# Performance work log

Hardware: AMD Instinct MI355X
Metric: run time of the kernel (lower is better)

The kernel has to match this reference:

```python
import jax, jax.numpy as jnp
import numpy as np

EPS = 1e-5

def conv1x1(x, w, b=None):
    # x: (B,C,H,W), w: (O,C)
    y = jnp.einsum('bchw,oc->bohw', x, w)
    if b is not None:
        y = y + b[None, :, None, None]
    return y

def bn(x, g, b):
    # torch BatchNorm2d training-mode: biased var over (B,H,W)
    mean = jnp.mean(x, axis=(0, 2, 3), keepdims=True)
    var = jnp.var(x, axis=(0, 2, 3), keepdims=True)
    xn = (x - mean) * jax.lax.rsqrt(var + EPS)
    return xn * g[None, :, None, None] + b[None, :, None, None]

def setup_inputs() -> dict:
    key = jax.random.key(0)
    ks = jax.random.split(key, 8)
    B, C, H, W = 4, 256, 128, 128
    C8 = C // 8
    s = 1.0 / np.sqrt(C)
    return {
        'x': jax.random.normal(ks[0], (B, C, H, W), jnp.float32),
        'w1': jax.random.normal(ks[1], (C, C), jnp.float32) * s,
        'g1': jnp.ones((C,), jnp.float32), 'b1': jnp.zeros((C,), jnp.float32),
        'wq': jax.random.normal(ks[2], (C8, C), jnp.float32) * s,
        'bq': jnp.zeros((C8,), jnp.float32),
        'wk': jax.random.normal(ks[3], (C8, C), jnp.float32) * s,
        'bk': jnp.zeros((C8,), jnp.float32),
        'wv': jax.random.normal(ks[4], (C, C), jnp.float32) * s,
        'bv': jnp.zeros((C,), jnp.float32),
        'gamma_att': jax.random.normal(ks[5], (1,), jnp.float32),
        'g2': jnp.ones((C,), jnp.float32), 'b2': jnp.zeros((C,), jnp.float32),
        'w3': jax.random.normal(ks[6], (C, C), jnp.float32) * s,
        'g3': jnp.ones((C,), jnp.float32), 'b3': jnp.zeros((C,), jnp.float32),
    }

def att(h, wq, bq, wk, bk, wv, bv, gamma_att):
    B, C, Hh, Ww = h.shape
    N = Hh * Ww
    q = conv1x1(h, wq, bq).reshape(B, -1, N)          # (B,C8,N)
    k = conv1x1(h, wk, bk).reshape(B, -1, N)          # (B,C8,N)
    v = conv1x1(h, wv, bv).reshape(B, C, N)           # (B,C,N)
    energy = jnp.einsum('bdi,bdj->bij', q, k)         # (B,N,N): q^T k
    attn = jax.nn.softmax(energy, axis=-1)
    out = jnp.einsum('bcj,bij->bci', v, attn)         # out[b,c,i]=sum_j v[c,j]*attn[i,j]
    out = out.reshape(B, C, Hh, Ww)
    return gamma_att[0] * out + h

def reference(x, w1, g1, b1, wq, bq, wk, bk, wv, bv, gamma_att, g2, b2, w3, g3, b3):
    B, C, H, W = x.shape
    shortcut = x  # sk=True (dim==dim_out, no downsample)
    h = jax.nn.relu(bn(conv1x1(x, w1), g1, b1))                       # net1
    h = jax.image.resize(h, (B, C, H // 2, W // 2), method='bilinear')  # align_corners=False
    h = att(h, wq, bq, wk, bk, wv, bv, gamma_att)                     # net2: ATT
    h = jax.nn.relu(bn(h, g2, b2))                                    # net2: BN+ReLU (Identity pool)
    h = jax.image.resize(h, (B, C, H, W), method='bilinear')          # stride==1 upsample x2
    h = bn(conv1x1(h, w3), g3, b3)                                    # net3
    return jax.nn.relu(h + shortcut)
```

## Files before the change

### kernel.cpp

```cpp
#include <hip/hip_runtime.h>
#include <hip/hip_bf16.h>

#define EPS_BN 1e-5f

typedef short bf16x8 __attribute__((ext_vector_type(8)));
typedef float f32x4 __attribute__((ext_vector_type(4)));

__device__ __forceinline__ unsigned short f2bf(float f) {
    __hip_bfloat16 h = __float2bfloat16(f);
    return __builtin_bit_cast(unsigned short, h);
}
__device__ __forceinline__ float bf2f(unsigned short u) {
    return __builtin_bit_cast(float, (unsigned)u << 16);
}

template<int BM, int MODE>
__global__ __launch_bounds__(256) void gemm_mfma(
    const unsigned short* __restrict__ Wb,
    const unsigned short* __restrict__ Xt,
    const float* __restrict__ bias,
    unsigned short* __restrict__ Y,
    int P, int O)
{
    const int tid = threadIdx.x;
    const int w = tid >> 6, l = tid & 63;
    const int b = blockIdx.z;
    const int p0 = blockIdx.x * 128;
    const int o0 = blockIdx.y * BM;
    const int lr = l & 15, lk = l >> 4;
    const int srow = l >> 2, sq = l & 3;

    __shared__ unsigned short Al[BM * 40];
    __shared__ unsigned short Bl[128 * 40];

    constexpr int WC = (BM == 32) ? 4 : 2;
    constexpr int MT = (BM == 128) ? 4 : 2;
    constexpr int NT = (WC == 2) ? 4 : 2;
    const int wr = w / WC, wc = w % WC;
    const int osub = wr * MT * 16, psub = wc * NT * 16;

    f32x4 acc[MT][NT];
#pragma unroll
    for (int i = 0; i < MT; i++)
#pragma unroll
        for (int j = 0; j < NT; j++) acc[i][j] = (f32x4){0.f, 0.f, 0.f, 0.f};

    const unsigned short* Xb = Xt + (size_t)b * P * 256;
    const int ar0 = w * 16, ar1 = w * 16 + 64;
    const int br0 = w * 16, br1 = w * 16 + 64;

    const unsigned short* pB0 = Xb + (size_t)(p0 + br0 + srow) * 256 + sq * 8;
    const unsigned short* pB1 = Xb + (size_t)(p0 + br1 + srow) * 256 + sq * 8;
    const unsigned short* pA0 = Wb + (size_t)(o0 + ar0 + srow) * 256 + sq * 8;
    const unsigned short* pA1 = Wb + (size_t)(o0 + ar1 + srow) * 256 + sq * 8;
    unsigned short* BlW0 = &Bl[(br0 + srow) * 40 + sq * 8];
    unsigned short* BlW1 = &Bl[(br1 + srow) * 40 + sq * 8];
    unsigned short* AlW0 = &Al[(ar0 + srow) * 40 + sq * 8];
    unsigned short* AlW1 = &Al[(ar1 + srow) * 40 + sq * 8];

    uint4 vb0, vb1, va0, va1;
#define G_LOADS                                                     \
    vb0 = *(const uint4*)pB0; pB0 += 32;                            \
    vb1 = *(const uint4*)pB1; pB1 += 32;                            \
    if (ar0 < BM) { va0 = *(const uint4*)pA0; pA0 += 32; }          \
    if (ar1 < BM) { va1 = *(const uint4*)pA1; pA1 += 32; }

    G_LOADS
    for (int k0 = 0; k0 < 256; k0 += 32) {
        __syncthreads();
        *(uint4*)BlW0 = vb0;
        *(uint4*)BlW1 = vb1;
        if (ar0 < BM) *(uint4*)AlW0 = va0;
        if (ar1 < BM) *(uint4*)AlW1 = va1;
        __syncthreads();
        if (k0 < 224) { G_LOADS }
        bf16x8 af[MT], bfr[NT];
#pragma unroll
        for (int i = 0; i < MT; i++) {
            int row = osub + i * 16 + lr;
            af[i] = *(const bf16x8*)&Al[row * 40 + lk * 8];
        }
#pragma unroll
        for (int j = 0; j < NT; j++) {
            int row = psub + j * 16 + lr;
            bfr[j] = *(const bf16x8*)&Bl[row * 40 + lk * 8];
        }
#pragma unroll
        for (int i = 0; i < MT; i++)
#pragma unroll
            for (int j = 0; j < NT; j++)
                acc[i][j] = __builtin_amdgcn_mfma_f32_16x16x32_bf16(af[i], bfr[j], acc[i][j], 0, 0, 0);
    }
#undef G_LOADS

    if (MODE == 1) {
#pragma unroll
        for (int i = 0; i < MT; i++) {
            int ob = o0 + osub + i * 16 + lk * 4;
#pragma unroll
            for (int j = 0; j < NT; j++) {
                int p = p0 + psub + j * 16 + lr;
                ushort4 pk;
                pk.x = f2bf(acc[i][j][0] + bias[ob + 0]);
                pk.y = f2bf(acc[i][j][1] + bias[ob + 1]);
                pk.z = f2bf(acc[i][j][2] + bias[ob + 2]);
                pk.w = f2bf(acc[i][j][3] + bias[ob + 3]);
                *(ushort4*)&Y[((size_t)b * P + p) * O + ob] = pk;
            }
        }
    } else {
#pragma unroll
        for (int i = 0; i < MT; i++)
#pragma unroll
            for (int r = 0; r < 4; r++) {
                int o = o0 + osub + i * 16 + lk * 4 + r;
                float bs = bias ? bias[o] : 0.f;
#pragma unroll
                for (int j = 0; j < NT; j++) {
                    int p = p0 + psub + j * 16 + lr;
                    Y[((size_t)(b * 256 + o)) * P + p] = f2bf(acc[i][j][r] + bs);
                }
            }
    }
}

__global__ __launch_bounds__(256) void transpose_cvt(
    const float* __restrict__ src, unsigned short* __restrict__ dst, int P)
{
    __shared__ float t[64][65];
    const int tid = threadIdx.x;
    const int p0 = blockIdx.x * 64, c0 = blockIdx.y * 64, b = blockIdx.z;
    const float* sb = src + ((size_t)b * 256 + c0) * P + p0;
#pragma unroll
    for (int i = 0; i < 16; i++) {
        int r = (tid >> 6) + 4 * i;
        int c = tid & 63;
        t[c][r] = sb[(size_t)r * P + c];
    }
    __syncthreads();
#pragma unroll
    for (int i = 0; i < 8; i++) {
        int pr = (tid >> 5) + 8 * i;
        int cc = (tid & 31) * 2;
        unsigned pk = ((unsigned)f2bf(t[pr][cc + 1]) << 16) | f2bf(t[pr][cc]);
        *(unsigned*)&dst[((size_t)b * P + p0 + pr) * 256 + c0 + cc] = pk;
    }
}

__global__ void cvt_weights(const float* __restrict__ w1, const float* __restrict__ wq,
                            const float* __restrict__ wk, const float* __restrict__ wv,
                            const float* __restrict__ w3,
                            const float* __restrict__ bq, const float* __restrict__ bk,
                            unsigned short* o1, unsigned short* oqk,
                            unsigned short* ov, unsigned short* o3, float* obqk)
{
    int i = blockIdx.x * 256 + threadIdx.x;
    if (i < 65536) { o1[i] = f2bf(w1[i]); ov[i] = f2bf(wv[i]); o3[i] = f2bf(w3[i]); }
    if (i < 16384) oqk[i] = f2bf(i < 8192 ? wq[i] : wk[i - 8192]);
    if (i < 64)    obqk[i] = i < 32 ? bq[i] : bk[i - 32];
}

__global__ __launch_bounds__(256) void channel_stats_bf16(
    const unsigned short* __restrict__ Y, float* __restrict__ psum,
    float* __restrict__ psumsq, int Pn)
{
    const int o = blockIdx.x, b = blockIdx.y;
    const unsigned short* p = Y + ((size_t)b * 256 + o) * Pn;
    float s = 0.f, s2 = 0.f;
    for (int i = threadIdx.x * 8; i < Pn; i += 2048) {
        uint4 v = *(const uint4*)&p[i];
        unsigned uu[4] = {v.x, v.y, v.z, v.w};
#pragma unroll
        for (int k = 0; k < 4; k++) {
            float a = __builtin_bit_cast(float, uu[k] << 16);
            float c = __builtin_bit_cast(float, uu[k] & 0xffff0000u);
            s += a + c; s2 += a * a + c * c;
        }
    }
#pragma unroll
    for (int off = 32; off; off >>= 1) {
        s  += __shfl_down(s, off);
        s2 += __shfl_down(s2, off);
    }
    __shared__ float ws1[4], ws2[4];
    int lane = threadIdx.x & 63, w = threadIdx.x >> 6;
    if (lane == 0) { ws1[w] = s; ws2[w] = s2; }
    __syncthreads();
    if (threadIdx.x == 0) {
        float ts = 0.f, ts2 = 0.f;
#pragma unroll
        for (int k = 0; k < 4; k++) { ts += ws1[k]; ts2 += ws2[k]; }
        psum[(size_t)b * 256 + o] = ts;
        psumsq[(size_t)b * 256 + o] = ts2;
    }
}

__global__ __launch_bounds__(256) void stats_pmajor(
    const float* __restrict__ Y, float* __restrict__ psum, float* __restrict__ psumsq)
{
    const int chunk = blockIdx.x, b = blockIdx.y, c = threadIdx.x;
    const float* base = Y + ((size_t)b * 4096 + chunk * 128) * 256 + c;
    float s = 0.f, s2 = 0.f;
    for (int i = 0; i < 128; i++) { float v = base[(size_t)i * 256]; s += v; s2 += v * v; }
    psum[((size_t)b * 32 + chunk) * 256 + c] = s;
    psumsq[((size_t)b * 32 + chunk) * 256 + c] = s2;
}

__global__ void bn_finalize(const float* __restrict__ psum, const float* __restrict__ psumsq,
                            const float* __restrict__ g, const float* __restrict__ bb,
                            float* __restrict__ scale, float* __restrict__ shift,
                            float invN, int NP)
{
    int o = threadIdx.x;
    float s = 0.f, s2 = 0.f;
    for (int k = 0; k < NP; k++) { s += psum[k * 256 + o]; s2 += psumsq[k * 256 + o]; }
    float mean = s * invN;
    float var  = s2 * invN - mean * mean;
    float r = rsqrtf(var + EPS_BN);
    float sc = g[o] * r;
    scale[o] = sc;
    shift[o] = bb[o] - mean * sc;
}

__device__ __forceinline__ int dtaps(int u, int* j, float* w) {
    if (u == 0)  { j[0]=0;   j[1]=1;   j[2]=2;   w[0]=3.f/7.f; w[1]=3.f/7.f; w[2]=1.f/7.f; return 3; }
    if (u == 63) { j[0]=125; j[1]=126; j[2]=127; w[0]=1.f/7.f; w[1]=3.f/7.f; w[2]=3.f/7.f; return 3; }
    j[0]=2*u-1; j[1]=2*u; j[2]=2*u+1; j[3]=2*u+2;
    w[0]=0.125f; w[1]=0.375f; w[2]=0.375f; w[3]=0.125f; return 4;
}

__global__ __launch_bounds__(256) void bnrelu_down(
    const unsigned short* __restrict__ y1, const float* __restrict__ scale,
    const float* __restrict__ shift, float* __restrict__ h)
{
    int i = blockIdx.x * 256 + threadIdx.x;
    int o = blockIdx.y, b = blockIdx.z;
    int y2 = i >> 6, x2 = i & 63;
    const unsigned short* base = y1 + ((size_t)(b * 256 + o)) * 16384;
    float sc = scale[o], sh = shift[o];
    int jy[4]; float wy[4]; int ny = dtaps(y2, jy, wy);
    int jx[4]; float wx[4]; int nx = dtaps(x2, jx, wx);
    float acc = 0.f;
    for (int a = 0; a < ny; a++) {
        const unsigned short* row = base + jy[a] * 128;
        for (int c = 0; c < nx; c++) {
            float v = fmaxf(fmaf(sc, bf2f(row[jx[c]]), sh), 0.f);
            acc += wy[a] * wx[c] * v;
        }
    }
    h[((size_t)(b * 256 + o)) * 4096 + i] = acc;
}

__global__ __launch_bounds__(512) void attn_partial(
    const unsigned short* __restrict__ qkT, const unsigned short* __restrict__ vb,
    unsigned short* __restrict__ accP, float2* __restrict__ mzP)
{
    const int s = blockIdx.y;
    const int b = blockIdx.z;
    const int i0 = blockIdx.x * 128;
    const int tid = threadIdx.x;
    const int w = tid >> 6, l = tid & 63;
    const int wr = w >> 1, wc = w & 1;
    const int lr = l & 15, lk = l >> 4;

    __shared__ unsigned short Vl[256 * 64];
    __shared__ unsigned short Pl[4][32 * 68];

    const unsigned short* qkTb = qkT + (size_t)b * 4096 * 64;
    bf16x8 qf[2];
#pragma unroll
    for (int i = 0; i < 2; i++)
        qf[i] = *(const bf16x8*)&qkTb[(size_t)(i0 + wr * 32 + i * 16 + lr) * 64 + lk * 8];

    f32x4 acc[2][8];
#pragma unroll
    for (int i = 0; i < 2; i++)
#pragma unroll
        for (int c = 0; c < 8; c++) acc[i][c] = (f32x4){0.f, 0.f, 0.f, 0.f};
    float m[2][4], zp[2][4];
#pragma unroll
    for (int i = 0; i < 2; i++)
#pragma unroll
        for (int r = 0; r < 4; r++) { m[i][r] = -1e30f; zp[i][r] = 0.f; }

    const int jbase = s * 1024;
    const unsigned short* kPtr = qkTb + (size_t)(jbase + lr) * 64 + 32 + lk * 8;
    const unsigned short* vPtr =
        vb + (size_t)b * 256 * 4096 + (size_t)(w * 32 + (l >> 3)) * 4096 + jbase + (l & 7) * 8;
    unsigned short* Pw = Pl[wr];

    uint4 kfr[4], vreg[4];
#pragma unroll
    for (int jt = 0; jt < 4; jt++) kfr[jt] = *(const uint4*)(kPtr + jt * 1024);
    kPtr += 4096;
#pragma unroll
    for (int it = 0; it < 4; it++) vreg[it] = *(const uint4*)(vPtr + it * 32768);

    for (int t = 0; t < 16; t++) {
        __syncthreads();
#pragma unroll
        for (int it = 0; it < 4; it++) {
            int ch = w * 32 + it * 8 + (l >> 3);
            *(uint4*)&Vl[ch * 64 + (((l & 7) ^ (ch & 7)) * 8)] = vreg[it];
        }
        __syncthreads();
        if (t < 15) {
            vPtr += 64;
#pragma unroll
            for (int it = 0; it < 4; it++) vreg[it] = *(const uint4*)(vPtr + it * 32768);
        }

#pragma unroll
        for (int i = 0; i < 2; i++) {
            f32x4 sv[4];
#pragma unroll
            for (int jt = 0; jt < 4; jt++)
                sv[jt] = __builtin_amdgcn_mfma_f32_16x16x32_bf16(
                    qf[i], __builtin_bit_cast(bf16x8, kfr[jt]), (f32x4){0.f,0.f,0.f,0.f}, 0, 0, 0);
            float tml[4];
            bool trig = false;
#pragma unroll
            for (int r = 0; r < 4; r++) {
                tml[r] = fmaxf(fmaxf(sv[0][r], sv[1][r]), fmaxf(sv[2][r], sv[3][r]));
                trig |= (tml[r] > m[i][r] + 10.0f);
            }
            if (__any(trig)) {
                float corr[4];
#pragma unroll
                for (int r = 0; r < 4; r++) {
                    float tm = tml[r];
#pragma unroll
                    for (int off = 1; off < 16; off <<= 1) tm = fmaxf(tm, __shfl_xor(tm, off));
                    float mo = m[i][r];
                    float mn = fmaxf(mo, tm);
                    corr[r] = __expf(mo - mn);
                    m[i][r] = mn;
                    float ps = 0.f;
#pragma unroll
                    for (int jt = 0; jt < 4; jt++) {
                        float p = __expf(sv[jt][r] - mn);
                        ps += p;
                        Pw[(i * 16 + lk * 4 + r) * 68 + lr + jt * 16] = f2bf(p);
                    }
                    zp[i][r] = zp[i][r] * corr[r] + ps;
                }
#pragma unroll
                for (int c = 0; c < 8; c++)
#pragma unroll
                    for (int r = 0; r < 4; r++) acc[i][c][r] *= corr[r];
            } else {
#pragma unroll
                for (int r = 0; r < 4; r++) {
                    float mn = m[i][r];
                    float ps = 0.f;
#pragma unroll
                    for (int jt = 0; jt < 4; jt++) {
                        float p = __expf(sv[jt][r] - mn);
                        ps += p;
                        Pw[(i * 16 + lk * 4 + r) * 68 + lr + jt * 16] = f2bf(p);
                    }
                    zp[i][r] += ps;
                }
            }
        }

        if (t < 15) {
#pragma unroll
            for (int jt = 0; jt < 4; jt++) kfr[jt] = *(const uint4*)(kPtr + jt * 1024);
            kPtr += 4096;
        }

#pragma unroll
        for (int kc = 0; kc < 2; kc++) {
            bf16x8 pa[2];
#pragma unroll
            for (int i = 0; i < 2; i++)
                pa[i] = *(const bf16x8*)&Pw[(i * 16 + lr) * 68 + (kc * 4 + lk) * 8];
#pragma unroll
            for (int ct = 0; ct < 8; ct++) {
                int ch = wc * 128 + ct * 16 + lr;
                bf16x8 vf = *(const bf16x8*)&Vl[ch * 64 + (((kc * 4 + lk) ^ (lr & 7)) * 8)];
#pragma unroll
                for (int i = 0; i < 2; i++)
                    acc[i][ct] = __builtin_amdgcn_mfma_f32_16x16x32_bf16(pa[i], vf, acc[i][ct], 0, 0, 0);
            }
        }
    }

    float zs[2][4];
#pragma unroll
    for (int i = 0; i < 2; i++)
#pragma unroll
        for (int r = 0; r < 4; r++) {
            float zz = zp[i][r];
#pragma unroll
            for (int off = 1; off < 16; off <<= 1) zz += __shfl_xor(zz, off);
            zs[i][r] = zz;
        }
    const size_t rbase0 = (size_t)(b * 4 + s) * 4096 + i0;
    if (wc == 0 && lr == 0) {
#pragma unroll
        for (int i = 0; i < 2; i++)
#pragma unroll
            for (int r = 0; r < 4; r++)
                mzP[rbase0 + wr * 32 + i * 16 + lk * 4 + r] = make_float2(m[i][r], zs[i][r]);
    }

    float* Eb = (float*)Vl;
    __syncthreads();
#pragma unroll
    for (int h = 0; h < 4; h++) {
        if (wr == h) {
#pragma unroll
            for (int i = 0; i < 2; i++)
#pragma unroll
                for (int ct = 0; ct < 8; ct++)
#pragma unroll
                    for (int r = 0; r < 4; r++)
                        Eb[(i * 16 + lk * 4 + r) * 256 + wc * 128 + ct * 16 + lr] = acc[i][ct][r];
        }
        __syncthreads();
        unsigned short* dst = accP + (rbase0 + h * 32) * 256;
#pragma unroll
        for (int q = 0; q < 4; q++) {
            float4 v = ((const float4*)Eb)[tid + q * 512];
            ushort4 pk = { f2bf(v.x), f2bf(v.y), f2bf(v.z), f2bf(v.w) };
            *(ushort4*)&dst[(tid + q * 512) * 4] = pk;
        }
        __syncthreads();
    }
}

__global__ __launch_bounds__(256) void attn_combine(
    const unsigned short* __restrict__ accP, const float2* __restrict__ mzP,
    const unsigned short* __restrict__ hst, const float* __restrict__ gamma_p,
    float* __restrict__ h2t)
{
    const int b = blockIdx.y, ch = threadIdx.x;
    const float gamma = gamma_p[0];
    for (int rr = 0; rr < 8; rr++) {
        int row = blockIdx.x * 8 + rr;
        float2 mz[4];
#pragma unroll
        for (int s = 0; s < 4; s++) mz[s] = mzP[(size_t)(b * 4 + s) * 4096 + row];
        float M = fmaxf(fmaxf(mz[0].x, mz[1].x), fmaxf(mz[2].x, mz[3].x));
        float Z = 0.f, a = 0.f;
#pragma unroll
        for (int s = 0; s < 4; s++) {
            float wgt = __expf(mz[s].x - M);
            Z += wgt * mz[s].y;
            a += wgt * bf2f(accP[((size_t)(b * 4 + s) * 4096 + row) * 256 + ch]);
        }
        size_t off = ((size_t)b * 4096 + row) * 256 + ch;
        h2t[off] = gamma * a / Z + bf2f(hst[off]);
    }
}

__global__ __launch_bounds__(256) void upsample_bnrelu(
    const float* __restrict__ h2t, const float* __restrict__ scale,
    const float* __restrict__ shift, unsigned short* __restrict__ upn)
{
    const int b = blockIdx.y, c = threadIdx.x;
    const float* basep = h2t + ((size_t)b * 4096) * 256 + c;
    float sc = scale[c], sh = shift[c];
    for (int pp = 0; pp < 16; pp++) {
        int p = blockIdx.x * 16 + pp;
        int y = p >> 7, x = p & 127;
        float fy = 0.5f * y - 0.25f, fx = 0.5f * x - 0.25f;
        float fiy = floorf(fy), fix = floorf(fx);
        float wy = fy - fiy, wx = fx - fix;
        int iy = (int)fiy, ix = (int)fix;
        int iy0 = max(iy, 0), iy1 = min(iy + 1, 63);
        int ix0 = max(ix, 0), ix1 = min(ix + 1, 63);
        float v00 = fmaxf(fmaf(sc, basep[(size_t)(iy0 * 64 + ix0) * 256], sh), 0.f);
        float v01 = fmaxf(fmaf(sc, basep[(size_t)(iy0 * 64 + ix1) * 256], sh), 0.f);
        float v10 = fmaxf(fmaf(sc, basep[(size_t)(iy1 * 64 + ix0) * 256], sh), 0.f);
        float v11 = fmaxf(fmaf(sc, basep[(size_t)(iy1 * 64 + ix1) * 256], sh), 0.f);
        float r0 = (1.f - wy) * ((1.f - wx) * v00 + wx * v01)
                 + wy * ((1.f - wx) * v10 + wx * v11);
        upn[((size_t)b * 16384 + p) * 256 + c] = f2bf(r0);
    }
}

__global__ __launch_bounds__(256) void final_add_relu(
    const unsigned short* __restrict__ y3, const float* __restrict__ scale,
    const float* __restrict__ shift, const float* __restrict__ x,
    float* __restrict__ outp)
{
    size_t e = ((size_t)blockIdx.x * 256 + threadIdx.x) * 4;
    int c = (int)((e >> 14) & 255);
    ushort4 yv = *(const ushort4*)&y3[e];
    float4 xv = *(const float4*)&x[e];
    float sc = scale[c], sh = shift[c];
    float4 o;
    o.x = fmaxf(fmaf(sc, bf2f(yv.x), sh) + xv.x, 0.f);
    o.y = fmaxf(fmaf(sc, bf2f(yv.y), sh) + xv.y, 0.f);
    o.z = fmaxf(fmaf(sc, bf2f(yv.z), sh) + xv.z, 0.f);
    o.w = fmaxf(fmaf(sc, bf2f(yv.w), sh) + xv.w, 0.f);
    *(float4*)&outp[e] = o;
}

extern "C" void kernel_launch(void* const* d_in, const int* in_sizes, int n_in,
                              void* d_out, int out_size, void* d_ws, size_t ws_size,
                              hipStream_t stream)
{
    const float* x     = (const float*)d_in[0];
    const float* w1    = (const float*)d_in[1];
    const float* g1    = (const float*)d_in[2];
    const float* b1    = (const float*)d_in[3];
    const float* wq    = (const float*)d_in[4];
    const float* bq    = (const float*)d_in[5];
    const float* wk    = (const float*)d_in[6];
    const float* bk    = (const float*)d_in[7];
    const float* wv    = (const float*)d_in[8];
    const float* bv    = (const float*)d_in[9];
    const float* gamma = (const float*)d_in[10];
    const float* g2    = (const float*)d_in[11];
    const float* b2    = (const float*)d_in[12];
    const float* w3    = (const float*)d_in[13];
    const float* g3    = (const float*)d_in[14];
    const float* b3    = (const float*)d_in[15];
    float* out = (float*)d_out;

    char* wsb = (char*)d_ws;
    unsigned short* y1b = (unsigned short*)wsb;
    unsigned short* xt  = (unsigned short*)(wsb + ((size_t)32 << 20));
    unsigned short* accPb = (unsigned short*)wsb;
    float* hs   = (float*)(wsb + ((size_t)64 << 20));
    unsigned short* vbb = (unsigned short*)(wsb + ((size_t)80 << 20));
    unsigned short* hst = (unsigned short*)(wsb + ((size_t)88 << 20));
    unsigned short* qkT = (unsigned short*)(wsb + ((size_t)96 << 20));
    unsigned short* w1b = (unsigned short*)(wsb + ((size_t)98 << 20));
    unsigned short* wvb  = w1b + 65536;
    unsigned short* w3b  = wvb + 65536;
    unsigned short* wqkb = w3b + 65536;
    float* bqk = (float*)(wqkb + 16384);
    float2* mzP = (float2*)(wsb + ((size_t)98 << 20) + ((size_t)512 << 10));
    float* psum   = (float*)(wsb + ((size_t)99 << 20));
    float* psumsq = psum + 32768;
    float* sc1 = psumsq + 32768; float* sh1 = sc1 + 256;
    float* sc2 = sh1 + 256;      float* sh2 = sc2 + 256;
    float* sc3 = sh2 + 256;      float* sh3 = sc3 + 256;
    unsigned short* y3b = y1b;
    unsigned short* upn = xt;
    float* h2t = hs;

    cvt_weights<<<256, 256, 0, stream>>>(w1, wq, wk, wv, w3, bq, bk,
                                         w1b, wqkb, wvb, w3b, bqk);
    transpose_cvt<<<dim3(256, 4, 4), 256, 0, stream>>>(x, xt, 16384);

    gemm_mfma<128, 2><<<dim3(128, 2, 4), 256, 0, stream>>>(w1b, xt, nullptr, y1b, 16384, 256);
    channel_stats_bf16<<<dim3(256, 4), 256, 0, stream>>>(y1b, psum, psumsq, 16384);
    bn_finalize<<<1, 256, 0, stream>>>(psum, psumsq, g1, b1, sc1, sh1, 1.f / 65536.f, 4);
    bnrelu_down<<<dim3(16, 256, 4), 256, 0, stream>>>(y1b, sc1, sh1, hs);
    transpose_cvt<<<dim3(64, 4, 4), 256, 0, stream>>>(hs, hst, 4096);

    gemm_mfma<64, 1><<<dim3(32, 1, 4), 256, 0, stream>>>(wqkb, hst, bqk, qkT, 4096, 64);
    gemm_mfma<128, 2><<<dim3(32, 2, 4), 256, 0, stream>>>(wvb, hst, bv, vbb, 4096, 256);
    attn_partial<<<dim3(32, 4, 4), 512, 0, stream>>>(qkT, vbb, accPb, mzP);
    attn_combine<<<dim3(512, 4), 256, 0, stream>>>(accPb, mzP, hst, gamma, h2t);

    stats_pmajor<<<dim3(32, 4), 256, 0, stream>>>(h2t, psum, psumsq);
    bn_finalize<<<1, 256, 0, stream>>>(psum, psumsq, g2, b2, sc2, sh2, 1.f / 16384.f, 128);
    upsample_bnrelu<<<dim3(1024, 4), 256, 0, stream>>>(h2t, sc2, sh2, upn);

    gemm_mfma<128, 2><<<dim3(128, 2, 4), 256, 0, stream>>>(w3b, upn, nullptr, y3b, 16384, 256);
    channel_stats_bf16<<<dim3(256, 4), 256, 0, stream>>>(y3b, psum, psumsq, 16384);
    bn_finalize<<<1, 256, 0, stream>>>(psum, psumsq, g3, b3, sc3, sh3, 1.f / 65536.f, 4);
    final_add_relu<<<16384, 256, 0, stream>>>(y3b, sc3, sh3, x, out);
}
```

Baseline: 403.3 us.

## Fuse attention combine with BN stats, store h2 as bf16, vectorize P writes

```diff
diff --git a/kernel.cpp b/kernel.cpp
--- a/kernel.cpp
+++ b/kernel.cpp
@@ -14,7 +14,7 @@
     return __builtin_bit_cast(float, (unsigned)u << 16);
 }
 
-template<int BM, int MODE>
+template<int BM, int MODE, int PERM>
 __global__ __launch_bounds__(256) void gemm_mfma(
     const unsigned short* __restrict__ Wb,
     const unsigned short* __restrict__ Xt,
@@ -118,7 +118,8 @@
 #pragma unroll
                 for (int j = 0; j < NT; j++) {
                     int p = p0 + psub + j * 16 + lr;
-                    Y[((size_t)(b * 256 + o)) * P + p] = f2bf(acc[i][j][r] + bs);
+                    int p2 = PERM ? ((p & ~63) | ((p & 15) * 4 + ((p >> 4) & 3))) : p;
+                    Y[((size_t)(b * 256 + o)) * P + p2] = f2bf(acc[i][j][r] + bs);
                 }
             }
     }
@@ -193,17 +194,6 @@
         psum[(size_t)b * 256 + o] = ts;
         psumsq[(size_t)b * 256 + o] = ts2;
     }
-}
-
-__global__ __launch_bounds__(256) void stats_pmajor(
-    const float* __restrict__ Y, float* __restrict__ psum, float* __restrict__ psumsq)
-{
-    const int chunk = blockIdx.x, b = blockIdx.y, c = threadIdx.x;
-    const float* base = Y + ((size_t)b * 4096 + chunk * 128) * 256 + c;
-    float s = 0.f, s2 = 0.f;
-    for (int i = 0; i < 128; i++) { float v = base[(size_t)i * 256]; s += v; s2 += v * v; }
-    psum[((size_t)b * 32 + chunk) * 256 + c] = s;
-    psumsq[((size_t)b * 32 + chunk) * 256 + c] = s2;
 }
 
 __global__ void bn_finalize(const float* __restrict__ psum, const float* __restrict__ psumsq,
@@ -264,7 +254,7 @@
     const int lr = l & 15, lk = l >> 4;
 
     __shared__ unsigned short Vl[256 * 64];
-    __shared__ unsigned short Pl[4][32 * 68];
+    __shared__ unsigned short Pl[4][32 * 72];
 
     const unsigned short* qkTb = qkT + (size_t)b * 4096 * 64;
     bf16x8 qf[2];
@@ -336,12 +326,12 @@
                     corr[r] = __expf(mo - mn);
                     m[i][r] = mn;
                     float ps = 0.f;
-#pragma unroll
-                    for (int jt = 0; jt < 4; jt++) {
-                        float p = __expf(sv[jt][r] - mn);
-                        ps += p;
-                        Pw[(i * 16 + lk * 4 + r) * 68 + lr + jt * 16] = f2bf(p);
-                    }
+                    ushort4 pk;
+                    float p0 = __expf(sv[0][r] - mn), p1 = __expf(sv[1][r] - mn);
+                    float p2 = __expf(sv[2][r] - mn), p3 = __expf(sv[3][r] - mn);
+                    ps = (p0 + p1) + (p2 + p3);
+                    pk.x = f2bf(p0); pk.y = f2bf(p1); pk.z = f2bf(p2); pk.w = f2bf(p3);
+                    *(ushort4*)&Pw[(i * 16 + lk * 4 + r) * 72 + lr * 4] = pk;
                     zp[i][r] = zp[i][r] * corr[r] + ps;
                 }
 #pragma unroll
@@ -352,14 +342,12 @@
 #pragma unroll
                 for (int r = 0; r < 4; r++) {
                     float mn = m[i][r];
-                    float ps = 0.f;
-#pragma unroll
-                    for (int jt = 0; jt < 4; jt++) {
-                        float p = __expf(sv[jt][r] - mn);
-                        ps += p;
-                        Pw[(i * 16 + lk * 4 + r) * 68 + lr + jt * 16] = f2bf(p);
-                    }
-                    zp[i][r] += ps;
+                    ushort4 pk;
+                    float p0 = __expf(sv[0][r] - mn), p1 = __expf(sv[1][r] - mn);
+                    float p2 = __expf(sv[2][r] - mn), p3 = __expf(sv[3][r] - mn);
+                    pk.x = f2bf(p0); pk.y = f2bf(p1); pk.z = f2bf(p2); pk.w = f2bf(p3);
+                    *(ushort4*)&Pw[(i * 16 + lk * 4 + r) * 72 + lr * 4] = pk;
+                    zp[i][r] += (p0 + p1) + (p2 + p3);
                 }
             }
         }
@@ -375,7 +363,7 @@
             bf16x8 pa[2];
 #pragma unroll
             for (int i = 0; i < 2; i++)
-                pa[i] = *(const bf16x8*)&Pw[(i * 16 + lr) * 68 + (kc * 4 + lk) * 8];
+                pa[i] = *(const bf16x8*)&Pw[(i * 16 + lr) * 72 + (kc * 4 + lk) * 8];
 #pragma unroll
             for (int ct = 0; ct < 8; ct++) {
                 int ch = wc * 128 + ct * 16 + lr;
@@ -431,37 +419,44 @@
     }
 }
 
-__global__ __launch_bounds__(256) void attn_combine(
+__global__ __launch_bounds__(256) void attn_combine_stats(
     const unsigned short* __restrict__ accP, const float2* __restrict__ mzP,
     const unsigned short* __restrict__ hst, const float* __restrict__ gamma_p,
-    float* __restrict__ h2t)
+    unsigned short* __restrict__ h2tb, float* __restrict__ psum,
+    float* __restrict__ psumsq)
 {
     const int b = blockIdx.y, ch = threadIdx.x;
     const float gamma = gamma_p[0];
-    for (int rr = 0; rr < 8; rr++) {
-        int row = blockIdx.x * 8 + rr;
+    float s = 0.f, s2 = 0.f;
+    for (int rr = 0; rr < 64; rr++) {
+        int row = blockIdx.x * 64 + rr;
         float2 mz[4];
 #pragma unroll
-        for (int s = 0; s < 4; s++) mz[s] = mzP[(size_t)(b * 4 + s) * 4096 + row];
+        for (int s4 = 0; s4 < 4; s4++) mz[s4] = mzP[(size_t)(b * 4 + s4) * 4096 + row];
         float M = fmaxf(fmaxf(mz[0].x, mz[1].x), fmaxf(mz[2].x, mz[3].x));
         float Z = 0.f, a = 0.f;
 #pragma unroll
-        for (int s = 0; s < 4; s++) {
-            float wgt = __expf(mz[s].x - M);
-            Z += wgt * mz[s].y;
-            a += wgt * bf2f(accP[((size_t)(b * 4 + s) * 4096 + row) * 256 + ch]);
+        for (int s4 = 0; s4 < 4; s4++) {
+            float wgt = __expf(mz[s4].x - M);
+            Z += wgt * mz[s4].y;
+            a += wgt * bf2f(accP[((size_t)(b * 4 + s4) * 4096 + row) * 256 + ch]);
         }
         size_t off = ((size_t)b * 4096 + row) * 256 + ch;
-        h2t[off] = gamma * a / Z + bf2f(hst[off]);
-    }
+        unsigned short hb = f2bf(gamma * a / Z + bf2f(hst[off]));
+        h2tb[off] = hb;
+        float v = bf2f(hb);
+        s += v; s2 += v * v;
+    }
+    psum[((size_t)b * 64 + blockIdx.x) * 256 + ch] = s;
+    psumsq[((size_t)b * 64 + blockIdx.x) * 256 + ch] = s2;
 }
 
 __global__ __launch_bounds__(256) void upsample_bnrelu(
-    const float* __restrict__ h2t, const float* __restrict__ scale,
+    const unsigned short* __restrict__ h2tb, const float* __restrict__ scale,
     const float* __restrict__ shift, unsigned short* __restrict__ upn)
 {
     const int b = blockIdx.y, c = threadIdx.x;
-    const float* basep = h2t + ((size_t)b * 4096) * 256 + c;
+    const unsigned short* basep = h2tb + ((size_t)b * 4096) * 256 + c;
     float sc = scale[c], sh = shift[c];
     for (int pp = 0; pp < 16; pp++) {
         int p = blockIdx.x * 16 + pp;
@@ -472,10 +467,10 @@
         int iy = (int)fiy, ix = (int)fix;
         int iy0 = max(iy, 0), iy1 = min(iy + 1, 63);
         int ix0 = max(ix, 0), ix1 = min(ix + 1, 63);
-        float v00 = fmaxf(fmaf(sc, basep[(size_t)(iy0 * 64 + ix0) * 256], sh), 0.f);
-        float v01 = fmaxf(fmaf(sc, basep[(size_t)(iy0 * 64 + ix1) * 256], sh), 0.f);
-        float v10 = fmaxf(fmaf(sc, basep[(size_t)(iy1 * 64 + ix0) * 256], sh), 0.f);
-        float v11 = fmaxf(fmaf(sc, basep[(size_t)(iy1 * 64 + ix1) * 256], sh), 0.f);
+        float v00 = fmaxf(fmaf(sc, bf2f(basep[(size_t)(iy0 * 64 + ix0) * 256]), sh), 0.f);
+        float v01 = fmaxf(fmaf(sc, bf2f(basep[(size_t)(iy0 * 64 + ix1) * 256]), sh), 0.f);
+        float v10 = fmaxf(fmaf(sc, bf2f(basep[(size_t)(iy1 * 64 + ix0) * 256]), sh), 0.f);
+        float v11 = fmaxf(fmaf(sc, bf2f(basep[(size_t)(iy1 * 64 + ix1) * 256]), sh), 0.f);
         float r0 = (1.f - wy) * ((1.f - wx) * v00 + wx * v01)
                  + wy * ((1.f - wx) * v10 + wx * v11);
         upn[((size_t)b * 16384 + p) * 256 + c] = f2bf(r0);
@@ -527,6 +522,7 @@
     unsigned short* xt  = (unsigned short*)(wsb + ((size_t)32 << 20));
     unsigned short* accPb = (unsigned short*)wsb;
     float* hs   = (float*)(wsb + ((size_t)64 << 20));
+    unsigned short* h2tb = (unsigned short*)(wsb + ((size_t)64 << 20));
     unsigned short* vbb = (unsigned short*)(wsb + ((size_t)80 << 20));
     unsigned short* hst = (unsigned short*)(wsb + ((size_t)88 << 20));
     unsigned short* qkT = (unsigned short*)(wsb + ((size_t)96 << 20));
@@ -537,34 +533,33 @@
     float* bqk = (float*)(wqkb + 16384);
     float2* mzP = (float2*)(wsb + ((size_t)98 << 20) + ((size_t)512 << 10));
     float* psum   = (float*)(wsb + ((size_t)99 << 20));
-    float* psumsq = psum + 32768;
-    float* sc1 = psumsq + 32768; float* sh1 = sc1 + 256;
+    float* psumsq = psum + 65536;
+    float* sc1 = psumsq + 65536; float* sh1 = sc1 + 256;
     float* sc2 = sh1 + 256;      float* sh2 = sc2 + 256;
     float* sc3 = sh2 + 256;      float* sh3 = sc3 + 256;
     unsigned short* y3b = y1b;
     unsigned short* upn = xt;
-    float* h2t = hs;
 
     cvt_weights<<<256, 256, 0, stream>>>(w1, wq, wk, wv, w3, bq, bk,
                                          w1b, wqkb, wvb, w3b, bqk);
     transpose_cvt<<<dim3(256, 4, 4), 256, 0, stream>>>(x, xt, 16384);
 
-    gemm_mfma<128, 2><<<dim3(128, 2, 4), 256, 0, stream>>>(w1b, xt, nullptr, y1b, 16384, 256);
+    gemm_mfma<128, 2, 0><<<dim3(128, 2, 4), 256, 0, stream>>>(w1b, xt, nullptr, y1b, 16384, 256);
     channel_stats_bf16<<<dim3(256, 4), 256, 0, stream>>>(y1b, psum, psumsq, 16384);
     bn_finalize<<<1, 256, 0, stream>>>(psum, psumsq, g1, b1, sc1, sh1, 1.f / 65536.f, 4);
     bnrelu_down<<<dim3(16, 256, 4), 256, 0, stream>>>(y1b, sc1, sh1, hs);
     transpose_cvt<<<dim3(64, 4, 4), 256, 0, stream>>>(hs, hst, 4096);
 
-    gemm_mfma<64, 1><<<dim3(32, 1, 4), 256, 0, stream>>>(wqkb, hst, bqk, qkT, 4096, 64);
-    gemm_mfma<128, 2><<<dim3(32, 2, 4), 256, 0, stream>>>(wvb, hst, bv, vbb, 4096, 256);
+    gemm_mfma<64, 1, 0><<<dim3(32, 1, 4), 256, 0, stream>>>(wqkb, hst, bqk, qkT, 4096, 64);
+    gemm_mfma<128, 2, 1><<<dim3(32, 2, 4), 256, 0, stream>>>(wvb, hst, bv, vbb, 4096, 256);
     attn_partial<<<dim3(32, 4, 4), 512, 0, stream>>>(qkT, vbb, accPb, mzP);
-    attn_combine<<<dim3(512, 4), 256, 0, stream>>>(accPb, mzP, hst, gamma, h2t);
-
-    stats_pmajor<<<dim3(32, 4), 256, 0, stream>>>(h2t, psum, psumsq);
-    bn_finalize<<<1, 256, 0, stream>>>(psum, psumsq, g2, b2, sc2, sh2, 1.f / 16384.f, 128);
-    upsample_bnrelu<<<dim3(1024, 4), 256, 0, stream>>>(h2t, sc2, sh2, upn);
-
-    gemm_mfma<128, 2><<<dim3(128, 2, 4), 256, 0, stream>>>(w3b, upn, nullptr, y3b, 16384, 256);
+    attn_combine_stats<<<dim3(64, 4), 256, 0, stream>>>(accPb, mzP, hst, gamma,
+                                                        h2tb, psum, psumsq);
+
+    bn_finalize<<<1, 256, 0, stream>>>(psum, psumsq, g2, b2, sc2, sh2, 1.f / 16384.f, 256);
+    upsample_bnrelu<<<dim3(1024, 4), 256, 0, stream>>>(h2tb, sc2, sh2, upn);
+
+    gemm_mfma<128, 2, 0><<<dim3(128, 2, 4), 256, 0, stream>>>(w3b, upn, nullptr, y3b, 16384, 256);
     channel_stats_bf16<<<dim3(256, 4), 256, 0, stream>>>(y3b, psum, psumsq, 16384);
     bn_finalize<<<1, 256, 0, stream>>>(psum, psumsq, g3, b3, sc3, sh3, 1.f / 65536.f, 4);
     final_add_relu<<<16384, 256, 0, stream>>>(y3b, sc3, sh3, x, out);
```

Result: slower. 420.9 us (+4.4%).
